# Kernel tuning notes

Measured on AMD Instinct MI355X. Metric: run time of the kernel, lower is better.

Reference implementation:

```python
import jax, jax.numpy as jnp
import numpy as np

B, S, D, H = 2, 2048, 1024, 16
HD = D // H


def setup_inputs() -> dict:
    key = jax.random.key(0)
    ks = jax.random.split(key, 7)
    mk = lambda k, shape, scale=1.0: (jax.random.normal(k, shape, dtype=jnp.float32) * scale)
    w_scale = 1.0 / np.sqrt(D)  # ~nn.Linear init scale
    return {
        "query": mk(ks[0], (B, S, D)),
        "key": mk(ks[1], (B, S, D)),
        "value": mk(ks[2], (B, S, D)),
        "Wq": mk(ks[3], (D, D), w_scale),
        "Wk": mk(ks[4], (D, D), w_scale),
        "Wv": mk(ks[5], (D, D), w_scale),
        "Wo": mk(ks[6], (D, D), w_scale),
    }


def reference(query, key, value, Wq, Wk, Wv, Wo):
    # torch nn.Linear(bias=False): y = x @ W.T, W is (out, in)
    def proj(x, W):
        y = jnp.einsum('bsd,ed->bse', x, W)          # [B, S, D]
        return y.reshape(x.shape[0], x.shape[1], H, HD).transpose(0, 2, 1, 3)  # [B, H, S, HD]

    Q = proj(query, Wq)
    K = proj(key, Wk)
    V = proj(value, Wv)

    # NOTE: original scales by sqrt(embedding_size), not sqrt(head_dim)
    scale = 1.0 / jnp.sqrt(jnp.asarray(D, dtype=Q.dtype))
    scores = jnp.einsum('bhqd,bhkd->bhqk', Q, K) * scale   # [B, H, Q, K]
    attn = jax.nn.softmax(scores, axis=-1)
    ctx = jnp.einsum('bhqk,bhkd->bhqd', attn, V)           # [B, H, Q, HD]
    ctx = ctx.transpose(0, 2, 1, 3).reshape(query.shape[0], query.shape[1], D)
    return jnp.einsum('bsd,ed->bse', ctx, Wo)
```

## Files before the change

kernel.cpp:

```cpp
#include <hip/hip_runtime.h>
#include <hip/hip_bf16.h>


typedef __bf16 bf16x8 __attribute__((ext_vector_type(8)));
typedef float f32x2 __attribute__((ext_vector_type(2)));
typedef float f32x4 __attribute__((ext_vector_type(4)));
typedef float f32x16 __attribute__((ext_vector_type(16)));
typedef int i32x4 __attribute__((ext_vector_type(4)));

static constexpr int Bb = 2, Ss = 2048, Dd = 1024, Hh = 16, HDd = 64;
static constexpr int Mtot = Bb * Ss;

__global__ __launch_bounds__(256) void cast_all(
    const float* __restrict__ a0, const float* __restrict__ a1, const float* __restrict__ a2,
    const float* __restrict__ a3, const float* __restrict__ a4, const float* __restrict__ a5,
    const float* __restrict__ a6, __hip_bfloat16* __restrict__ d0, __hip_bfloat16* __restrict__ d1,
    __hip_bfloat16* __restrict__ d2, __hip_bfloat16* __restrict__ d3,
    __hip_bfloat16* __restrict__ d4, __hip_bfloat16* __restrict__ d5,
    __hip_bfloat16* __restrict__ d6, int nact8, int nw8) {
  const float* src;
  __hip_bfloat16* dst;
  int n8;
  switch (blockIdx.y) {
    case 0: src = a0; dst = d0; n8 = nact8; break;
    case 1: src = a1; dst = d1; n8 = nact8; break;
    case 2: src = a2; dst = d2; n8 = nact8; break;
    case 3: src = a3; dst = d3; n8 = nw8; break;
    case 4: src = a4; dst = d4; n8 = nw8; break;
    case 5: src = a5; dst = d5; n8 = nw8; break;
    default: src = a6; dst = d6; n8 = nw8; break;
  }
  int i = blockIdx.x * 256 + threadIdx.x;
  if (i >= n8) return;
  const float4* s4 = (const float4*)src + (size_t)i * 2;
  float4 a = s4[0], b = s4[1];
  union { __hip_bfloat16 h[8]; int4 v; } u;
  u.h[0] = __float2bfloat16(a.x); u.h[1] = __float2bfloat16(a.y);
  u.h[2] = __float2bfloat16(a.z); u.h[3] = __float2bfloat16(a.w);
  u.h[4] = __float2bfloat16(b.x); u.h[5] = __float2bfloat16(b.y);
  u.h[6] = __float2bfloat16(b.z); u.h[7] = __float2bfloat16(b.w);
  ((int4*)dst)[i] = u.v;
}

#define BM 128
#define BK 64

__device__ __forceinline__ void gload_lds16(const void* g, void* l) {
  __builtin_amdgcn_global_load_lds((const __attribute__((address_space(1))) unsigned*)g,
                                   (__attribute__((address_space(3))) unsigned*)l, 16, 0, 0);
}

__device__ __forceinline__ void storeC(float* C, size_t idx, float v) { C[idx] = v; }
__device__ __forceinline__ void storeC(__hip_bfloat16* C, size_t idx, float v) {
  C[idx] = __float2bfloat16(v);
}

template <typename OutT, int BNT>
__device__ __forceinline__ void gemm_bt_body(const __hip_bfloat16* __restrict__ A,
                                             const __hip_bfloat16* __restrict__ Bw,
                                             OutT* __restrict__ C, int K, int N, float cscale,
                                             int bm, int bn) {
  constexpr int NTC = BNT / 32;
  __shared__ __hip_bfloat16 As[BM * BK];
  __shared__ __hip_bfloat16 Bs[BNT * BK];
  const int tid = threadIdx.x;
  const int lane = tid & 63;
  const int wid = tid >> 6;
  const int wm = (wid >> 1) * 64;
  const int wn = (wid & 1) * (BNT / 2);
  const int l15 = lane & 15;
  const int lhi = lane >> 4;

  f32x4 zero = {0.f, 0.f, 0.f, 0.f};
  f32x4 acc[4][NTC];
#pragma unroll
  for (int i = 0; i < 4; ++i)
#pragma unroll
    for (int j = 0; j < NTC; ++j) acc[i][j] = zero;

  const size_t abase = (size_t)(bm * BM) * K;
  const size_t bbase = (size_t)(bn * BNT) * K;

  for (int k0 = 0; k0 < K; k0 += BK) {
#pragma unroll
    for (int p = 0; p < 4; ++p) {
      int c = p * 256 + tid;
      int row = c >> 3;
      int col = (c & 7) * 8;
      gload_lds16(A + abase + (size_t)row * K + k0 + col, (char*)As + c * 16);
    }
#pragma unroll
    for (int p = 0; p < BNT / 32; ++p) {
      int c = p * 256 + tid;
      int row = c >> 3;
      int col = (c & 7) * 8;
      gload_lds16(Bw + bbase + (size_t)row * K + k0 + col, (char*)Bs + c * 16);
    }
    __syncthreads();
#pragma unroll
    for (int kk = 0; kk < 2; ++kk) {
      bf16x8 af[4], bfr[NTC];
#pragma unroll
      for (int mt = 0; mt < 4; ++mt)
        af[mt] = *(const bf16x8*)&As[(wm + mt * 16 + l15) * BK + kk * 32 + lhi * 8];
#pragma unroll
      for (int nt = 0; nt < NTC; ++nt)
        bfr[nt] = *(const bf16x8*)&Bs[(wn + nt * 16 + l15) * BK + kk * 32 + lhi * 8];
#pragma unroll
      for (int mt = 0; mt < 4; ++mt)
#pragma unroll
        for (int nt = 0; nt < NTC; ++nt)
          acc[mt][nt] = __builtin_amdgcn_mfma_f32_16x16x32_bf16(af[mt], bfr[nt], acc[mt][nt], 0, 0, 0);
    }
    __syncthreads();
  }

#pragma unroll
  for (int mt = 0; mt < 4; ++mt)
#pragma unroll
    for (int r = 0; r < 4; ++r) {
      int row = bm * BM + wm + mt * 16 + lhi * 4 + r;
#pragma unroll
      for (int nt = 0; nt < NTC; ++nt) {
        int col = bn * BNT + wn + nt * 16 + l15;
        storeC(C, (size_t)row * N + col, acc[mt][nt][r] * cscale);
      }
    }
}

__global__ __launch_bounds__(256) void qkv_proj(
    const __hip_bfloat16* __restrict__ xq, const __hip_bfloat16* __restrict__ xk,
    const __hip_bfloat16* __restrict__ xv, const __hip_bfloat16* __restrict__ wq,
    const __hip_bfloat16* __restrict__ wk, const __hip_bfloat16* __restrict__ wv,
    __hip_bfloat16* __restrict__ Qp, __hip_bfloat16* __restrict__ Kp,
    __hip_bfloat16* __restrict__ Vp) {
  const __hip_bfloat16* A;
  const __hip_bfloat16* W;
  __hip_bfloat16* C;
  float cs = 1.0f;
  if (blockIdx.z == 0) { A = xq; W = wq; C = Qp; cs = 0.04508422f; }
  else if (blockIdx.z == 1) { A = xk; W = wk; C = Kp; }
  else { A = xv; W = wv; C = Vp; }
  gemm_bt_body<__hip_bfloat16, 128>(A, W, C, Dd, Dd, cs, blockIdx.x, blockIdx.y);
}

__global__ __launch_bounds__(256) void out_proj(const __hip_bfloat16* __restrict__ ctx,
                                                const __hip_bfloat16* __restrict__ wo,
                                                float* __restrict__ out) {
  const int bid = blockIdx.x;
  const int wsw = (bid & 7) * 64 + (bid >> 3);
  const int bm = wsw >> 4, bn = wsw & 15;
  gemm_bt_body<float, 64>(ctx, wo, out, Dd, Dd, 1.0f, bm, bn);
}

__global__ __launch_bounds__(256) void transpose_v(const __hip_bfloat16* __restrict__ Vp,
                                                   __hip_bfloat16* __restrict__ Vt) {
  __shared__ __hip_bfloat16 T[64][72];
  const int tid = threadIdx.x;
  const int s0 = blockIdx.x * 64;
  const int bh = blockIdx.y;
  const int b = bh >> 4, h = bh & 15;
  const __hip_bfloat16* src = Vp + (size_t)b * Ss * Dd + (size_t)h * HDd;
#pragma unroll
  for (int p = 0; p < 2; ++p) {
    int id = p * 256 + tid;
    int r = id >> 3, c8 = (id & 7) * 8;
    *(int4*)&T[r][c8] = *(const int4*)(src + (size_t)(s0 + r) * Dd + c8);
  }
  __syncthreads();
#pragma unroll
  for (int p = 0; p < 2; ++p) {
    int id = p * 256 + tid;
    int d = id >> 3, s8 = (id & 7) * 8;
    union { int4 v; __hip_bfloat16 hh[8]; } u;
#pragma unroll
    for (int j = 0; j < 8; ++j) u.hh[j] = T[s8 + j][d];
    *(int4*)(Vt + ((size_t)bh * HDd + d) * Ss + s0 + s8) = u.v;
  }
}

__global__ __launch_bounds__(256, 4) void attn_kernel(const __hip_bfloat16* __restrict__ Qp,
                                                      const __hip_bfloat16* __restrict__ Kp,
                                                      const __hip_bfloat16* __restrict__ Vt,
                                                      float* __restrict__ Po,
                                                      float* __restrict__ Pl) {
  constexpr int HT = 16;
  __shared__ __align__(16) __hip_bfloat16 Ks[2][64 * 64];
  __shared__ __align__(16) __hip_bfloat16 Vs[2][64 * 64];

  const int tid = threadIdx.x;
  const int lane = tid & 63, wid = tid >> 6;
  const int l31 = lane & 31;
  const bool hih = (lane >= 32);
  const int lhi2 = hih ? 1 : 0;

  const int bid = blockIdx.x;
  const int w = (bid & 7) * 128 + (bid >> 3);
  const int bh = w >> 5;
  const int qblk = (w & 31) >> 1;
  const int half = w & 1;

  const int b = bh >> 4, h = bh & 15;
  const size_t head_off = (size_t)b * Ss * Dd + (size_t)h * HDd;
  const size_t vt_off = (size_t)bh * HDd * Ss;
  const int qrow = qblk * 128 + wid * 32 + l31;

  bf16x8 qf[4];
#pragma unroll
  for (int ksd = 0; ksd < 4; ++ksd)
    qf[ksd] = *(const bf16x8*)(Qp + head_off + (size_t)qrow * Dd + ksd * 16 + lhi2 * 8);

  const i32x4 onesbits = {0x3F803F80, 0x3F803F80, 0x3F803F80, 0x3F803F80};
  const bf16x8 ones = __builtin_bit_cast(bf16x8, onesbits);

  f32x16 o[2], ol, fz;
#pragma unroll
  for (int r = 0; r < 16; ++r) { o[0][r] = 0.f; o[1][r] = 0.f; ol[r] = 0.f; fz[r] = 0.f; }

  auto stage_K = [&](int buf, int kv0) {
#pragma unroll
    for (int p = 0; p < 2; ++p) {
      int c = p * 256 + tid;
      int row = c >> 3;
      int sch = (c & 7) ^ (row & 7);
      gload_lds16(Kp + head_off + (size_t)(kv0 + row) * Dd + sch * 8,
                  (char*)&Ks[buf][0] + c * 16);
    }
  };
  auto stage_V = [&](int buf, int kv0) {
#pragma unroll
    for (int p = 0; p < 2; ++p) {
      int c = p * 256 + tid;
      int row = c >> 3;
      int sch = (c & 7) ^ (row & 7);
      gload_lds16(Vt + vt_off + (size_t)row * Ss + kv0 + sch * 8,
                  (char*)&Vs[buf][0] + c * 16);
    }
  };

  const int t0 = half * HT;
  stage_K(0, (t0 + 0) * 64);
  stage_V(0, (t0 + 0) * 64);
  stage_K(1, (t0 + 1) * 64);
  stage_V(1, (t0 + 1) * 64);
  asm volatile("s_waitcnt vmcnt(4)" ::: "memory");
  __builtin_amdgcn_s_barrier();
  __builtin_amdgcn_sched_barrier(0);

  for (int t = 0; t < HT; ++t) {
    const int cur = t & 1;
    if (t > 0 && t + 1 < HT) {
      stage_K(cur ^ 1, (t0 + t + 1) * 64);
      stage_V(cur ^ 1, (t0 + t + 1) * 64);
    }

    const char* kbase = (const char*)&Ks[cur][0];
    bf16x8 kfrag[2][4];
#pragma unroll
    for (int kb = 0; kb < 2; ++kb) {
      int row = kb * 32 + l31;
#pragma unroll
      for (int ksd = 0; ksd < 4; ++ksd)
        kfrag[kb][ksd] = *(const bf16x8*)(kbase + row * 128 +
                                          (((ksd * 2 + lhi2) ^ (row & 7)) << 4));
    }
    f32x16 st[2];
    __builtin_amdgcn_s_setprio(1);
#pragma unroll
    for (int kb = 0; kb < 2; ++kb) {
      st[kb] = __builtin_amdgcn_mfma_f32_32x32x16_bf16(kfrag[kb][0], qf[0], fz, 0, 0, 0);
#pragma unroll
      for (int ksd = 1; ksd < 4; ++ksd)
        st[kb] = __builtin_amdgcn_mfma_f32_32x32x16_bf16(kfrag[kb][ksd], qf[ksd], st[kb], 0, 0, 0);
    }
    __builtin_amdgcn_s_setprio(0);

#pragma unroll
    for (int kb = 0; kb < 2; ++kb)
#pragma unroll
      for (int r = 0; r < 16; ++r) st[kb][r] = exp2f(st[kb][r]);

    int cpk[2][4][2];
#pragma unroll
    for (int kb = 0; kb < 2; ++kb)
#pragma unroll
      for (int g = 0; g < 4; ++g)
#pragma unroll
        for (int i = 0; i < 2; ++i) {
          int rr;
          float lo = st[kb][g * 4 + 2 * i], hi = st[kb][g * 4 + 2 * i + 1];
          asm("v_cvt_pk_bf16_f32 %0, %1, %2" : "=v"(rr) : "v"(lo), "v"(hi));
          cpk[kb][g][i] = rr;
        }

    if (t + 1 < HT) {
      asm volatile("s_waitcnt vmcnt(4)" ::: "memory");
    } else {
      asm volatile("s_waitcnt vmcnt(0)" ::: "memory");
    }

    const char* vbase = (const char*)&Vs[cur][0];
    bf16x8 vfrag[4][2];
#pragma unroll
    for (int ks = 0; ks < 4; ++ks)
#pragma unroll
      for (int db = 0; db < 2; ++db) {
        int row = db * 32 + l31;
        vfrag[ks][db] = *(const bf16x8*)(vbase + row * 128 +
                                         (((ks * 2 + lhi2) ^ (row & 7)) << 4));
      }
    __builtin_amdgcn_s_setprio(1);
#pragma unroll
    for (int ks = 0; ks < 4; ++ks) {
      const int kb = ks >> 1, m = ks & 1;
      int w0, w1, w2, w3;
#if __has_builtin(__builtin_amdgcn_permlane32_swap)
      {
        auto r0 = __builtin_amdgcn_permlane32_swap(cpk[kb][2 * m][0], cpk[kb][2 * m + 1][0],
                                                   false, false);
        auto r1 = __builtin_amdgcn_permlane32_swap(cpk[kb][2 * m][1], cpk[kb][2 * m + 1][1],
                                                   false, false);
        w0 = r0[0]; w2 = r0[1];
        w1 = r1[0]; w3 = r1[1];
      }
#else
      {
        int cA0 = cpk[kb][2 * m][0], cB0 = cpk[kb][2 * m + 1][0];
        int cA1 = cpk[kb][2 * m][1], cB1 = cpk[kb][2 * m + 1][1];
        int pay0 = hih ? cA0 : cB0, own0 = hih ? cB0 : cA0;
        int pay1 = hih ? cA1 : cB1, own1 = hih ? cB1 : cA1;
        int rcv0 = __shfl_xor(pay0, 32);
        int rcv1 = __shfl_xor(pay1, 32);
        w0 = hih ? rcv0 : own0;
        w1 = hih ? rcv1 : own1;
        w2 = hih ? own0 : rcv0;
        w3 = hih ? own1 : rcv1;
      }
#endif
      i32x4 bw = {w0, w1, w2, w3};
      bf16x8 pfrag = __builtin_bit_cast(bf16x8, bw);
#pragma unroll
      for (int db = 0; db < 2; ++db)
        o[db] = __builtin_amdgcn_mfma_f32_32x32x16_bf16(vfrag[ks][db], pfrag, o[db], 0, 0, 0);
      ol = __builtin_amdgcn_mfma_f32_32x32x16_bf16(ones, pfrag, ol, 0, 0, 0);
    }
    __builtin_amdgcn_s_setprio(0);

    if (t + 1 < HT) {
      asm volatile("s_waitcnt vmcnt(2)" ::: "memory");
      __builtin_amdgcn_s_barrier();
      __builtin_amdgcn_sched_barrier(0);
    }
  }

  const int qlocal = wid * 32 + l31;
  float* prow = Po + (size_t)w * (128 * 64) + (size_t)qlocal * 64;
#pragma unroll
  for (int db = 0; db < 2; ++db)
#pragma unroll
    for (int g = 0; g < 4; ++g) {
      f32x4 v4 = {o[db][g * 4 + 0], o[db][g * 4 + 1], o[db][g * 4 + 2], o[db][g * 4 + 3]};
      *(f32x4*)(prow + db * 32 + 8 * g + 4 * lhi2) = v4;
    }
  if (!hih) Pl[(size_t)w * 128 + qlocal] = ol[0];
}

__global__ __launch_bounds__(256) void merge_halves(const float* __restrict__ Po,
                                                    const float* __restrict__ Pl,
                                                    __hip_bfloat16* __restrict__ ctx) {
  const int mb = blockIdx.x;
  const int bh = mb >> 4, qblk = mb & 15;
  const int b = bh >> 4, h = bh & 15;
  const int tid = threadIdx.x;
  const size_t w0 = ((size_t)bh * 16 + qblk) * 2;
  const float* base = Po + w0 * 8192;
  const float* lbase = Pl + w0 * 128;
  __hip_bfloat16* cbase = ctx + (size_t)b * Ss * Dd + (size_t)(qblk * 128) * Dd + h * HDd;

#pragma unroll
  for (int it = 0; it < 8; ++it) {
    int c = it * 256 + tid;
    int q = c >> 4;
    int d0 = (c & 15) * 4;
    f32x4 v0 = *(const f32x4*)(base + (size_t)q * 64 + d0);
    f32x4 v1 = *(const f32x4*)(base + 8192 + (size_t)q * 64 + d0);
    float l = lbase[q] + lbase[128 + q];
    f32x4 s = (v0 + v1) * (1.f / l);
    union { uint2 uv; __hip_bfloat16 hh[4]; } u;
#pragma unroll
    for (int k = 0; k < 4; ++k) u.hh[k] = __float2bfloat16(s[k]);
    *(uint2*)(cbase + (size_t)q * Dd + d0) = u.uv;
  }
}

extern "C" void kernel_launch(void* const* d_in, const int* in_sizes, int n_in,
                              void* d_out, int out_size, void* d_ws, size_t ws_size,
                              hipStream_t stream) {
  const float* q_f = (const float*)d_in[0];
  const float* k_f = (const float*)d_in[1];
  const float* v_f = (const float*)d_in[2];
  const float* wq_f = (const float*)d_in[3];
  const float* wk_f = (const float*)d_in[4];
  const float* wv_f = (const float*)d_in[5];
  const float* wo_f = (const float*)d_in[6];
  float* out = (float*)d_out;

  const size_t act = (size_t)Mtot * Dd;
  const size_t wsz = (size_t)Dd * Dd;
  char* ws = (char*)d_ws;

  __hip_bfloat16* Qp = (__hip_bfloat16*)ws;   ws += act * 2;
  __hip_bfloat16* Kp = (__hip_bfloat16*)ws;   ws += act * 2;
  __hip_bfloat16* Vt = (__hip_bfloat16*)ws;   ws += act * 2;
  __hip_bfloat16* ctxb = (__hip_bfloat16*)ws; ws += act * 2;
  __hip_bfloat16* wob = (__hip_bfloat16*)ws;  ws += wsz * 2;

  char* scratch = ws;
  __hip_bfloat16* qb = (__hip_bfloat16*)scratch;
  __hip_bfloat16* kb = qb + act;
  __hip_bfloat16* vb = kb + act;
  __hip_bfloat16* wqb = vb + act;
  __hip_bfloat16* wkb = wqb + wsz;
  __hip_bfloat16* wvb = wkb + wsz;
  __hip_bfloat16* Vp = wvb + wsz;

  float* Po = (float*)scratch;
  float* Pl = Po + (size_t)1024 * 128 * 64;

  dim3 gc((unsigned)(act / 8 / 256), 7);
  cast_all<<<gc, 256, 0, stream>>>(q_f, k_f, v_f, wq_f, wk_f, wv_f, wo_f, qb, kb, vb, wqb,
                                   wkb, wvb, wob, (int)(act / 8), (int)(wsz / 8));

  dim3 gq(Mtot / BM, Dd / 128, 3);
  qkv_proj<<<gq, 256, 0, stream>>>(qb, kb, vb, wqb, wkb, wvb, Qp, Kp, Vp);

  dim3 gt(Ss / 64, Bb * Hh);
  transpose_v<<<gt, 256, 0, stream>>>(Vp, Vt);

  attn_kernel<<<1024, 256, 0, stream>>>(Qp, Kp, Vt, Po, Pl);

  merge_halves<<<512, 256, 0, stream>>>(Po, Pl, ctxb);

  out_proj<<<512, 256, 0, stream>>>(ctxb, wob, out);
}
```

Baseline: 154.9 us.

## Fuse V transpose into V projection epilogue and compact cast grid

V is now projected by its own GEMM kernel whose epilogue writes straight into the head-transposed Vt layout, so the separate transpose kernel and its intermediate Vp buffer are gone. The cast kernel now uses a flat 1D grid sized exactly to the activation and weight chunks, instead of a 7-row grid where most weight rows exited early. The transposed epilogue does 8-byte stores strided by the sequence length, which may coalesce worse than row-major stores. Q/K and V are now two launches instead of one.

```diff
diff --git a/kernel.cpp b/kernel.cpp
--- a/kernel.cpp
+++ b/kernel.cpp
@@ -17,21 +17,23 @@
     const float* __restrict__ a6, __hip_bfloat16* __restrict__ d0, __hip_bfloat16* __restrict__ d1,
     __hip_bfloat16* __restrict__ d2, __hip_bfloat16* __restrict__ d3,
     __hip_bfloat16* __restrict__ d4, __hip_bfloat16* __restrict__ d5,
-    __hip_bfloat16* __restrict__ d6, int nact8, int nw8) {
+    __hip_bfloat16* __restrict__ d6) {
+  const int bid = blockIdx.x;
   const float* src;
   __hip_bfloat16* dst;
-  int n8;
-  switch (blockIdx.y) {
-    case 0: src = a0; dst = d0; n8 = nact8; break;
-    case 1: src = a1; dst = d1; n8 = nact8; break;
-    case 2: src = a2; dst = d2; n8 = nact8; break;
-    case 3: src = a3; dst = d3; n8 = nw8; break;
-    case 4: src = a4; dst = d4; n8 = nw8; break;
-    case 5: src = a5; dst = d5; n8 = nw8; break;
-    default: src = a6; dst = d6; n8 = nw8; break;
+  int i;
+  if (bid < 6144) {
+    int a = bid >> 11;
+    src = (a == 0) ? a0 : (a == 1) ? a1 : a2;
+    dst = (a == 0) ? d0 : (a == 1) ? d1 : d2;
+    i = (bid & 2047) * 256 + threadIdx.x;
+  } else {
+    int r = bid - 6144;
+    int a = r >> 9;
+    src = (a == 0) ? a3 : (a == 1) ? a4 : (a == 2) ? a5 : a6;
+    dst = (a == 0) ? d3 : (a == 1) ? d4 : (a == 2) ? d5 : d6;
+    i = (r & 511) * 256 + threadIdx.x;
   }
-  int i = blockIdx.x * 256 + threadIdx.x;
-  if (i >= n8) return;
   const float4* s4 = (const float4*)src + (size_t)i * 2;
   float4 a = s4[0], b = s4[1];
   union { __hip_bfloat16 h[8]; int4 v; } u;
@@ -55,7 +57,7 @@
   C[idx] = __float2bfloat16(v);
 }
 
-template <typename OutT, int BNT>
+template <typename OutT, int BNT, bool VT>
 __device__ __forceinline__ void gemm_bt_body(const __hip_bfloat16* __restrict__ A,
                                              const __hip_bfloat16* __restrict__ Bw,
                                              OutT* __restrict__ C, int K, int N, float cscale,
@@ -115,33 +117,55 @@
     __syncthreads();
   }
 
-#pragma unroll
-  for (int mt = 0; mt < 4; ++mt)
-#pragma unroll
-    for (int r = 0; r < 4; ++r) {
-      int row = bm * BM + wm + mt * 16 + lhi * 4 + r;
+  if constexpr (VT) {
+    const int b = bm >> 4;
+    const int sbase = (bm & 15) * 128 + wm;
+#pragma unroll
+    for (int mt = 0; mt < 4; ++mt) {
+      int s0 = sbase + mt * 16 + lhi * 4;
 #pragma unroll
       for (int nt = 0; nt < NTC; ++nt) {
         int col = bn * BNT + wn + nt * 16 + l15;
-        storeC(C, (size_t)row * N + col, acc[mt][nt][r] * cscale);
+        int bh = b * 16 + (col >> 6);
+        int hd = col & 63;
+        union { uint2 v; __hip_bfloat16 hh[4]; } u;
+#pragma unroll
+        for (int r = 0; r < 4; ++r) u.hh[r] = __float2bfloat16(acc[mt][nt][r] * cscale);
+        *(uint2*)((__hip_bfloat16*)C + ((size_t)bh * HDd + hd) * (size_t)Ss + s0) = u.v;
       }
     }
+  } else {
+#pragma unroll
+    for (int mt = 0; mt < 4; ++mt)
+#pragma unroll
+      for (int r = 0; r < 4; ++r) {
+        int row = bm * BM + wm + mt * 16 + lhi * 4 + r;
+#pragma unroll
+        for (int nt = 0; nt < NTC; ++nt) {
+          int col = bn * BNT + wn + nt * 16 + l15;
+          storeC(C, (size_t)row * N + col, acc[mt][nt][r] * cscale);
+        }
+      }
+  }
 }
 
 __global__ __launch_bounds__(256) void qkv_proj(
     const __hip_bfloat16* __restrict__ xq, const __hip_bfloat16* __restrict__ xk,
-    const __hip_bfloat16* __restrict__ xv, const __hip_bfloat16* __restrict__ wq,
-    const __hip_bfloat16* __restrict__ wk, const __hip_bfloat16* __restrict__ wv,
-    __hip_bfloat16* __restrict__ Qp, __hip_bfloat16* __restrict__ Kp,
-    __hip_bfloat16* __restrict__ Vp) {
+    const __hip_bfloat16* __restrict__ wq, const __hip_bfloat16* __restrict__ wk,
+    __hip_bfloat16* __restrict__ Qp, __hip_bfloat16* __restrict__ Kp) {
   const __hip_bfloat16* A;
   const __hip_bfloat16* W;
   __hip_bfloat16* C;
   float cs = 1.0f;
   if (blockIdx.z == 0) { A = xq; W = wq; C = Qp; cs = 0.04508422f; }
-  else if (blockIdx.z == 1) { A = xk; W = wk; C = Kp; }
-  else { A = xv; W = wv; C = Vp; }
-  gemm_bt_body<__hip_bfloat16, 128>(A, W, C, Dd, Dd, cs, blockIdx.x, blockIdx.y);
+  else { A = xk; W = wk; C = Kp; }
+  gemm_bt_body<__hip_bfloat16, 128, false>(A, W, C, Dd, Dd, cs, blockIdx.x, blockIdx.y);
+}
+
+__global__ __launch_bounds__(256) void v_proj(const __hip_bfloat16* __restrict__ xv,
+                                              const __hip_bfloat16* __restrict__ wv,
+                                              __hip_bfloat16* __restrict__ Vt) {
+  gemm_bt_body<__hip_bfloat16, 128, true>(xv, wv, Vt, Dd, Dd, 1.0f, blockIdx.x, blockIdx.y);
 }
 
 __global__ __launch_bounds__(256) void out_proj(const __hip_bfloat16* __restrict__ ctx,
@@ -150,33 +174,7 @@
   const int bid = blockIdx.x;
   const int wsw = (bid & 7) * 64 + (bid >> 3);
   const int bm = wsw >> 4, bn = wsw & 15;
-  gemm_bt_body<float, 64>(ctx, wo, out, Dd, Dd, 1.0f, bm, bn);
-}
-
-__global__ __launch_bounds__(256) void transpose_v(const __hip_bfloat16* __restrict__ Vp,
-                                                   __hip_bfloat16* __restrict__ Vt) {
-  __shared__ __hip_bfloat16 T[64][72];
-  const int tid = threadIdx.x;
-  const int s0 = blockIdx.x * 64;
-  const int bh = blockIdx.y;
-  const int b = bh >> 4, h = bh & 15;
-  const __hip_bfloat16* src = Vp + (size_t)b * Ss * Dd + (size_t)h * HDd;
-#pragma unroll
-  for (int p = 0; p < 2; ++p) {
-    int id = p * 256 + tid;
-    int r = id >> 3, c8 = (id & 7) * 8;
-    *(int4*)&T[r][c8] = *(const int4*)(src + (size_t)(s0 + r) * Dd + c8);
-  }
-  __syncthreads();
-#pragma unroll
-  for (int p = 0; p < 2; ++p) {
-    int id = p * 256 + tid;
-    int d = id >> 3, s8 = (id & 7) * 8;
-    union { int4 v; __hip_bfloat16 hh[8]; } u;
-#pragma unroll
-    for (int j = 0; j < 8; ++j) u.hh[j] = T[s8 + j][d];
-    *(int4*)(Vt + ((size_t)bh * HDd + d) * Ss + s0 + s8) = u.v;
-  }
+  gemm_bt_body<float, 64, false>(ctx, wo, out, Dd, Dd, 1.0f, bm, bn);
 }
 
 __global__ __launch_bounds__(256, 4) void attn_kernel(const __hip_bfloat16* __restrict__ Qp,
@@ -422,20 +420,18 @@
   __hip_bfloat16* wqb = vb + act;
   __hip_bfloat16* wkb = wqb + wsz;
   __hip_bfloat16* wvb = wkb + wsz;
-  __hip_bfloat16* Vp = wvb + wsz;
 
   float* Po = (float*)scratch;
   float* Pl = Po + (size_t)1024 * 128 * 64;
 
-  dim3 gc((unsigned)(act / 8 / 256), 7);
-  cast_all<<<gc, 256, 0, stream>>>(q_f, k_f, v_f, wq_f, wk_f, wv_f, wo_f, qb, kb, vb, wqb,
-                                   wkb, wvb, wob, (int)(act / 8), (int)(wsz / 8));
-
-  dim3 gq(Mtot / BM, Dd / 128, 3);
-  qkv_proj<<<gq, 256, 0, stream>>>(qb, kb, vb, wqb, wkb, wvb, Qp, Kp, Vp);
-
-  dim3 gt(Ss / 64, Bb * Hh);
-  transpose_v<<<gt, 256, 0, stream>>>(Vp, Vt);
+  cast_all<<<8192, 256, 0, stream>>>(q_f, k_f, v_f, wq_f, wk_f, wv_f, wo_f, qb, kb, vb, wqb,
+                                     wkb, wvb, wob);
+
+  dim3 gq(Mtot / BM, Dd / 128, 2);
+  qkv_proj<<<gq, 256, 0, stream>>>(qb, kb, wqb, wkb, Qp, Kp);
+
+  dim3 gv(Mtot / BM, Dd / 128);
+  v_proj<<<gv, 256, 0, stream>>>(vb, wvb, Vt);
 
   attn_kernel<<<1024, 256, 0, stream>>>(Qp, Kp, Vt, Po, Pl);
 
```

Measured after the change: 154.7 us. No clear change (-0.1%).
